# Optimization experiments

Measured on AMD Instinct MI355X. Metric: run time of the kernel, lower is better.

The kernel has to match this reference:

```python
import jax, jax.numpy as jnp
import numpy as np

B, D, H, W, C = 2, 8, 128, 128, 64
HEADS, DH = 4, 16
EPS = 1e-12  # torch F.normalize eps


def setup_inputs() -> dict:
    key = jax.random.key(0)
    ks = jax.random.split(key, 8)
    rn = lambda k, shp, s: jax.random.normal(k, shp, jnp.float32) * s
    return {
        "x_in": rn(ks[0], (B, D, H, W, C), 1.0),
        "Wq": rn(ks[1], (C, HEADS * DH), 0.05),
        "Wk": rn(ks[2], (C, HEADS * DH), 0.05),
        "Wv": rn(ks[3], (C, HEADS * DH), 0.05),
        "rescale": jnp.ones((HEADS, 1, 1), jnp.float32),
        "Wproj": rn(ks[4], (HEADS * DH, C), 0.05),
        "bproj": jnp.zeros((C,), jnp.float32),
        "Wpos1": rn(ks[5], (C, 1, 3, 3, 3), 0.1),
        "Wpos2": rn(ks[6], (C, 1, 3, 3, 3), 0.1),
    }


def _l2norm(x):
    # torch F.normalize(p=2, dim=-1): x / max(||x||, eps)
    return x / jnp.maximum(jnp.linalg.norm(x, axis=-1, keepdims=True), EPS)


def _dwconv3d(x, w):
    # depthwise Conv3d, kernel 3, stride 1, padding 1, groups = channels
    return jax.lax.conv_general_dilated(
        x, w, (1, 1, 1), 'SAME',
        dimension_numbers=('NCDHW', 'OIDHW', 'NCDHW'),
        feature_group_count=w.shape[0])


def reference(x_in, Wq, Wk, Wv, rescale, Wproj, bproj, Wpos1, Wpos2):
    b, d, h, w, c = x_in.shape
    n = d * h * w
    x = x_in.reshape(b, n, c)
    v_inp = x @ Wv                                   # [b, n, heads*dh]
    # [b, heads, dh, n] layout (attention over channel dim)
    q = jnp.transpose((x @ Wq).reshape(b, n, HEADS, DH), (0, 2, 3, 1))
    k = jnp.transpose((x @ Wk).reshape(b, n, HEADS, DH), (0, 2, 3, 1))
    v = jnp.transpose(v_inp.reshape(b, n, HEADS, DH), (0, 2, 3, 1))
    q = _l2norm(q)
    k = _l2norm(k)
    attn = jnp.einsum('bhdn,bhen->bhde', k, q) * rescale  # [b, heads, dh, dh]
    attn = jax.nn.softmax(attn, axis=-1)
    out = jnp.einsum('bhde,bhen->bhdn', attn, v)          # [b, heads, dh, n]
    out = jnp.transpose(out, (0, 3, 1, 2)).reshape(b, n, HEADS * DH)
    out_c = (out @ Wproj + bproj).reshape(b, d, h, w, c)
    # positional branch: depthwise conv -> GELU -> depthwise conv on v_inp
    vv = jnp.transpose(v_inp.reshape(b, d, h, w, c), (0, 4, 1, 2, 3))  # NCDHW
    p = _dwconv3d(vv, Wpos1)
    p = jax.nn.gelu(p, approximate=False)
    p = _dwconv3d(p, Wpos2)
    out_p = jnp.transpose(p, (0, 2, 3, 4, 1))
    return out_c + out_p
```

## Files before the change

### kernel.cpp

```cpp
#include <hip/hip_runtime.h>
#include <math.h>

#define DD 8
#define HH 128
#define WW2 128
#define NPT 131072
#define NTOT 262144
#define NBK 8

typedef __attribute__((ext_vector_type(8))) short short8;
typedef __attribute__((ext_vector_type(4))) float f32x4;
typedef __attribute__((ext_vector_type(4))) unsigned short u16x4;
typedef __attribute__((ext_vector_type(8))) unsigned short u16x8;
typedef unsigned short u16;

static const size_t OFF_P1  = 0;
static const size_t OFF_P2  = 33554432;
static const size_t OFF_V   = 67108864;
static const size_t OFF_PW  = 100663296;
static const size_t OFF_PM  = 100687872;
static const size_t OFF_FLAG= 100704256;
static const size_t OFF_CW  = 100704768;
static const size_t OFF_PART= 134217728;
static const size_t OFF_VP  = 150994944;
#define SP_F    0
#define WQ_F    65536
#define WK_F    69632
#define CW_WPROJ 0
#define CW_WPOS1 4096
#define CW_WPOS2 5824
#define CW_RESC  7552
#define CW_BPROJ 7556

__device__ __forceinline__ float bf2f(u16 u){
  unsigned int x = ((unsigned int)u) << 16;
  return __builtin_bit_cast(float, x);
}
__device__ __forceinline__ u16 f2bf(float f){
  unsigned int x = __builtin_bit_cast(unsigned int, f);
  unsigned int r = (x + 0x7fffu + ((x >> 16) & 1u)) >> 16;
  return (u16)r;
}

__device__ __forceinline__ float fgelu(float o){
  float z  = o * 0.70710678118654752f;
  float az = fabsf(z);
  float t1 = __builtin_amdgcn_rcpf(fmaf(0.3275911f, az, 1.f));
  float poly = t1 * fmaf(t1, fmaf(t1, fmaf(t1, fmaf(t1, 1.061405429f,
               -1.453152027f), 1.421413741f), -0.284496736f), 0.254829592f);
  float ex = __expf(-z * z);
  float er = 1.f - poly * ex;
  er = (z < 0.f) ? -er : er;
  return 0.5f * o * (1.f + er);
}

__device__ __forceinline__ int probe_isf32(const void* x, int t){
  u16 u = ((const u16*)x)[2 * (t & 63)];
  int e = (u >> 7) & 0xFF;
  int plaus = (u == 0) || (u == 0x8000u) || (e >= 100 && e <= 130);
  unsigned long long m = __ballot(plaus);
  return (__popcll(m) < 48) ? 1 : 0;
}

__global__ __launch_bounds__(256) void k_prep(const void* __restrict__ x,
    const void* __restrict__ Wproj, const void* __restrict__ rescale,
    const void* __restrict__ bproj, const void* __restrict__ Wpos1,
    const void* __restrict__ Wpos2, const void* __restrict__ Wq,
    const void* __restrict__ Wk, const void* __restrict__ Wv,
    int* __restrict__ flag, float* __restrict__ cw, float* __restrict__ gpart,
    u16* __restrict__ packW){
  __shared__ int sflag;
  int t = threadIdx.x, blk = blockIdx.x;
  if (t < 64){
    int f = probe_isf32(x, t);
    if (t == 0) sflag = f;
  }
  __syncthreads();
  int isf32 = sflag;
  if (blk < 32){
    for (int i = blk * 2048 + t; i < (blk + 1) * 2048; i += 256)
      gpart[i] = 0.f;
    if (blk == 0){
      if (t == 0) *flag = isf32;
      auto conv = [&](const void* src, float* dst, int n){
        for (int i = t; i < n; i += 256)
          dst[i] = isf32 ? ((const float*)src)[i] : bf2f(((const u16*)src)[i]);
      };
      conv(Wproj, cw + CW_WPROJ, 4096);
      conv(Wpos1, cw + CW_WPOS1, 1728);
      conv(Wpos2, cw + CW_WPOS2, 1728);
      conv(rescale, cw + CW_RESC, 4);
      conv(bproj,   cw + CW_BPROJ, 64);
      conv(Wq, gpart + WQ_F, 4096);
      conv(Wk, gpart + WK_F, 4096);
    }
  } else {
    int o = (blk - 32) * 256 + t;
    int f = o >> 9, l = (o >> 3) & 63, j = o & 7;
    int tt = f >> 1, s = f & 1;
    int k = s * 32 + (l >> 4) * 8 + j;
    int n = tt * 16 + (l & 15);
    int idx = k * 64 + n;
    float val = isf32 ? ((const float*)Wv)[idx] : bf2f(((const u16*)Wv)[idx]);
    packW[o] = f2bf(val);
  }
}

__device__ __forceinline__ short8 ld8_adapt(const void* p, size_t idx, int isf32){
  if (!isf32) return *(const short8*)((const u16*)p + idx);
  const float4* f = (const float4*)((const float*)p + idx);
  float4 u = f[0], v2 = f[1];
  short8 r;
  r[0] = (short)f2bf(u.x);  r[1] = (short)f2bf(u.y);
  r[2] = (short)f2bf(u.z);  r[3] = (short)f2bf(u.w);
  r[4] = (short)f2bf(v2.x); r[5] = (short)f2bf(v2.y);
  r[6] = (short)f2bf(v2.z); r[7] = (short)f2bf(v2.w);
  return r;
}

__global__ __launch_bounds__(512) void k_qkv(const void* __restrict__ x,
                                             const int* __restrict__ flag,
                                             const u16* __restrict__ packW,
                                             u16* __restrict__ vT,
                                             u16* __restrict__ vP,
                                             float* __restrict__ Sp){
  __shared__ u16 sXT[64][136];
  int isf32 = *flag;
  int wave = threadIdx.x >> 6, lane = threadIdx.x & 63;
  int m = lane & 15, quad = lane >> 4;
  const short8* bw = (const short8*)packW;
  short8 bv[8];
#pragma unroll
  for (int f = 0; f < 8; f++) bv[f] = bw[f * 64 + lane];
  int c1 = wave >> 1, c2p = (wave & 1) * 2;
  f32x4 aS[2];
  aS[0] = (f32x4)(0.f); aS[1] = (f32x4)(0.f);

  int pbase = blockIdx.x * 512;
  int b = pbase >> 17;

  for (int s = 0; s < 4; s++){
    int p0 = pbase + s * 128 + wave * 16;
    size_t rowbase = (size_t)(p0 + m) * 64;
    short8 a0 = ld8_adapt(x, rowbase + quad * 8, isf32);
    short8 a1 = ld8_adapt(x, rowbase + 32 + quad * 8, isf32);
    f32x4 av[4];
#pragma unroll
    for (int t = 0; t < 4; t++) av[t] = (f32x4)(0.f);
#pragma unroll
    for (int t = 0; t < 4; t++){
      av[t] = __builtin_amdgcn_mfma_f32_16x16x32_bf16(a0, bv[t * 2 + 0], av[t], 0, 0, 0);
      av[t] = __builtin_amdgcn_mfma_f32_16x16x32_bf16(a1, bv[t * 2 + 1], av[t], 0, 0, 0);
    }
    int nloc = p0 & (NPT - 1);
#pragma unroll
    for (int t = 0; t < 4; t++){
      u16x4 pk;
#pragma unroll
      for (int r = 0; r < 4; r++) pk[r] = f2bf(av[t][r]);
      *(u16x4*)(vT + ((size_t)(b * 64 + t * 16 + m)) * NPT + nloc + quad * 4) = pk;
#pragma unroll
      for (int r = 0; r < 4; r++)
        vP[(size_t)(p0 + quad * 4 + r) * 64 + t * 16 + m] = pk[r];
    }
    if (s) __syncthreads();
#pragma unroll
    for (int j = 0; j < 8; j++){
      sXT[quad * 8 + j][wave * 16 + m]      = (u16)a0[j];
      sXT[32 + quad * 8 + j][wave * 16 + m] = (u16)a1[j];
    }
    __syncthreads();
#pragma unroll
    for (int ks = 0; ks < 4; ks++){
      short8 fA  = *(const short8*)&sXT[c1 * 16 + m][ks * 32 + quad * 8];
      short8 fB0 = *(const short8*)&sXT[(c2p + 0) * 16 + m][ks * 32 + quad * 8];
      short8 fB1 = *(const short8*)&sXT[(c2p + 1) * 16 + m][ks * 32 + quad * 8];
      aS[0] = __builtin_amdgcn_mfma_f32_16x16x32_bf16(fA, fB0, aS[0], 0, 0, 0);
      aS[1] = __builtin_amdgcn_mfma_f32_16x16x32_bf16(fA, fB1, aS[1], 0, 0, 0);
    }
  }
  int bk = blockIdx.x & (NBK - 1);
  float* Sb = Sp + (size_t)(bk * 2 + b) * 4096;
#pragma unroll
  for (int tt = 0; tt < 2; tt++)
#pragma unroll
    for (int r = 0; r < 4; r++)
      atomicAdd(&Sb[(c1 * 16 + quad * 4 + r) * 64 + (c2p + tt) * 16 + m], aS[tt][r]);
}

__global__ __launch_bounds__(256) void k_attn_h(const float* __restrict__ Sp,
    const float* __restrict__ wqk, const float* __restrict__ cw,
    u16* __restrict__ packM){
  __shared__ float sS[64 * 65];
  __shared__ float sWh[1024];
  __shared__ float sT[1024];
  __shared__ float sG[256];
  __shared__ float sA[256];
  __shared__ float sNq[16], sNk[16];
  int blk = blockIdx.x, t = threadIdx.x;
  int b = blk >> 2, h = blk & 3;
  for (int i = t; i < 4096; i += 256){
    float s = 0.f;
#pragma unroll
    for (int bk = 0; bk < NBK; bk++) s += Sp[(size_t)(bk * 2 + b) * 4096 + i];
    sS[(i >> 6) * 65 + (i & 63)] = s;
  }
  for (int i = t; i < 1024; i += 256)
    sWh[i] = wqk[(i >> 4) * 64 + h * 16 + (i & 15)];
  __syncthreads();
  int cc = t & 63, eg = t >> 6;
  {
    float a0 = 0.f, a1 = 0.f, a2 = 0.f, a3 = 0.f;
    for (int c2 = 0; c2 < 64; c2++){
      float sv = sS[cc * 65 + c2];
      a0 = fmaf(sv, sWh[c2 * 16 + eg * 4 + 0], a0);
      a1 = fmaf(sv, sWh[c2 * 16 + eg * 4 + 1], a1);
      a2 = fmaf(sv, sWh[c2 * 16 + eg * 4 + 2], a2);
      a3 = fmaf(sv, sWh[c2 * 16 + eg * 4 + 3], a3);
    }
    sT[cc * 16 + eg * 4 + 0] = a0;
    sT[cc * 16 + eg * 4 + 1] = a1;
    sT[cc * 16 + eg * 4 + 2] = a2;
    sT[cc * 16 + eg * 4 + 3] = a3;
  }
  __syncthreads();
  if (t < 16){
    float a = 0.f;
    for (int c = 0; c < 64; c++) a += sWh[c * 16 + t] * sT[c * 16 + t];
    sNq[t] = a;
  }
  __syncthreads();
  for (int i = t; i < 1024; i += 256)
    sWh[i] = wqk[4096 + (i >> 4) * 64 + h * 16 + (i & 15)];
  __syncthreads();
  {
    int d = t >> 4, e = t & 15;
    float a = 0.f;
    for (int c = 0; c < 64; c++) a += sWh[c * 16 + d] * sT[c * 16 + e];
    sG[d * 16 + e] = a;
  }
  __syncthreads();
  {
    float a0 = 0.f, a1 = 0.f, a2 = 0.f, a3 = 0.f;
    for (int c2 = 0; c2 < 64; c2++){
      float sv = sS[cc * 65 + c2];
      a0 = fmaf(sv, sWh[c2 * 16 + eg * 4 + 0], a0);
      a1 = fmaf(sv, sWh[c2 * 16 + eg * 4 + 1], a1);
      a2 = fmaf(sv, sWh[c2 * 16 + eg * 4 + 2], a2);
      a3 = fmaf(sv, sWh[c2 * 16 + eg * 4 + 3], a3);
    }
    __syncthreads();
    sT[cc * 16 + eg * 4 + 0] = a0;
    sT[cc * 16 + eg * 4 + 1] = a1;
    sT[cc * 16 + eg * 4 + 2] = a2;
    sT[cc * 16 + eg * 4 + 3] = a3;
  }
  __syncthreads();
  if (t < 16){
    float a = 0.f;
    for (int c = 0; c < 64; c++) a += sWh[c * 16 + t] * sT[c * 16 + t];
    sNk[t] = a;
  }
  __syncthreads();
  for (int i = t; i < 1024; i += 256)
    sT[i] = cw[CW_WPROJ + (h * 16 + (i >> 6)) * 64 + (i & 63)];
  if (t < 16){
    int d = t;
    float nk = fmaxf(sqrtf(sNk[d]), 1e-12f);
    float rs = cw[CW_RESC + h];
    float lg[16]; float mx = -1e30f;
#pragma unroll
    for (int e = 0; e < 16; e++){
      float nq = fmaxf(sqrtf(sNq[e]), 1e-12f);
      float L = sG[d * 16 + e] / (nk * nq) * rs;
      lg[e] = L; mx = fmaxf(mx, L);
    }
    float sum = 0.f;
#pragma unroll
    for (int e = 0; e < 16; e++){ lg[e] = expf(lg[e] - mx); sum += lg[e]; }
    float inv = 1.f / sum;
#pragma unroll
    for (int e = 0; e < 16; e++) sA[d * 16 + e] = lg[e] * inv;
  }
  __syncthreads();
#pragma unroll
  for (int q = 0; q < 4; q++){
    int i = q * 256 + t;
    int t4 = i >> 8, lhi = (i >> 7) & 1, llo = (i >> 3) & 15, j = i & 7;
    int e = lhi * 8 + j, c = t4 * 16 + llo;
    float acc = 0.f;
#pragma unroll
    for (int d = 0; d < 16; d++) acc += sA[d * 16 + e] * sT[d * 64 + c];
    int f = t4 * 2 + (h >> 1);
    int l = (2 * (h & 1) + lhi) * 16 + llo;
    packM[b * 4096 + f * 512 + l * 8 + j] = f2bf(acc);
  }
}

template <bool GELU>
__global__ __launch_bounds__(256, 3) void k_dwconv(const u16* __restrict__ src,
    const float* __restrict__ wpos, u16* __restrict__ dst){
  int xi = threadIdx.x & 15, ty = threadIdx.x >> 4;
  int zp = ty >> 2, yq = ty & 3;
  int x0 = xi * 8;
  int c  = blockIdx.x;
  int y0 = blockIdx.y * 8 + yq * 2;
  int b  = blockIdx.z;
  int z0 = zp * 2;
  const float* wg = wpos + c * 27;
  float w27[27];
#pragma unroll
  for (int i = 0; i < 27; i++) w27[i] = wg[i];
  const u16* plane = src + (size_t)(b * 64 + c) * NPT;

  short8 raw[16];
  float  msk[16];
#pragma unroll
  for (int iz = 0; iz < 4; iz++){
    int zz = z0 - 1 + iz;
    int zc = zz < 0 ? 0 : (zz > DD - 1 ? DD - 1 : zz);
    float zm = (zz == zc) ? 1.f : 0.f;
#pragma unroll
    for (int iy = 0; iy < 4; iy++){
      int yy = y0 - 1 + iy;
      int yc = yy < 0 ? 0 : (yy > HH - 1 ? HH - 1 : yy);
      raw[iz * 4 + iy] = *(const short8*)(plane + zc * 16384 + yc * 128 + x0);
      msk[iz * 4 + iy] = zm * ((yy == yc) ? 1.f : 0.f);
    }
  }

  float acc[2][2][8];
#pragma unroll
  for (int dz = 0; dz < 2; dz++)
#pragma unroll
    for (int dy = 0; dy < 2; dy++)
#pragma unroll
      for (int xx = 0; xx < 8; xx++) acc[dz][dy][xx] = 0.f;

#pragma unroll
  for (int iz = 0; iz < 4; iz++){
#pragma unroll
    for (int iy = 0; iy < 4; iy++){
      short8 mid = raw[iz * 4 + iy];
      float m = msk[iz * 4 + iy];
      float row[10];
#pragma unroll
      for (int e = 0; e < 8; e++) row[1 + e] = bf2f((u16)mid[e]);
      float lf = __shfl_up(row[8], 1);
      float rg = __shfl_down(row[1], 1);
      row[0] = (xi > 0)  ? lf : 0.f;
      row[9] = (xi < 15) ? rg : 0.f;
#pragma unroll
      for (int e = 0; e < 10; e++) row[e] *= m;
#pragma unroll
      for (int dzi = 0; dzi < 2; dzi++){
        int kd = iz - dzi;
        if (kd < 0 || kd > 2) continue;
#pragma unroll
        for (int dyi = 0; dyi < 2; dyi++){
          int kh = iy - dyi;
          if (kh < 0 || kh > 2) continue;
#pragma unroll
          for (int kw = 0; kw < 3; kw++){
            float w = w27[kd * 9 + kh * 3 + kw];
#pragma unroll
            for (int xx = 0; xx < 8; xx++)
              acc[dzi][dyi][xx] = fmaf(row[xx + kw], w, acc[dzi][dyi][xx]);
          }
        }
      }
    }
  }
#pragma unroll
  for (int dzi = 0; dzi < 2; dzi++){
    int zo = z0 + dzi;
#pragma unroll
    for (int dyi = 0; dyi < 2; dyi++){
      int yo = y0 + dyi;
      u16x8 pk;
#pragma unroll
      for (int xx = 0; xx < 8; xx++){
        float o = acc[dzi][dyi][xx];
        if (GELU) o = fgelu(o);
        pk[xx] = f2bf(o);
      }
      *(u16x8*)(dst + (size_t)(b * 64 + c) * NPT + zo * 16384 + yo * 128 + x0) = pk;
    }
  }
}

__global__ __launch_bounds__(256) void k_final(const u16* __restrict__ vP,
                                               const u16* __restrict__ packM,
                                               const float* __restrict__ bprojf,
                                               const u16* __restrict__ p2T,
                                               float* __restrict__ out){
  int wave = threadIdx.x >> 6, lane = threadIdx.x & 63;
  int m = lane & 15, quad = lane >> 4;
  int p0 = blockIdx.x * 64 + wave * 16;
  int b = p0 >> 17;
  int nloc = p0 & (NPT - 1);
  size_t rowbase = (size_t)(p0 + m) * 64;
  short8 a0 = *(const short8*)(vP + rowbase + quad * 8);
  short8 a1 = *(const short8*)(vP + rowbase + 32 + quad * 8);
  const short8* bm = (const short8*)(packM + (size_t)b * 4096);
  f32x4 acc[4];
#pragma unroll
  for (int t = 0; t < 4; t++) acc[t] = (f32x4)(0.f);
#pragma unroll
  for (int t = 0; t < 4; t++){
    short8 b0 = bm[(t * 2 + 0) * 64 + lane];
    short8 b1 = bm[(t * 2 + 1) * 64 + lane];
    acc[t] = __builtin_amdgcn_mfma_f32_16x16x32_bf16(a0, b0, acc[t], 0, 0, 0);
    acc[t] = __builtin_amdgcn_mfma_f32_16x16x32_bf16(a1, b1, acc[t], 0, 0, 0);
  }
#pragma unroll
  for (int t = 0; t < 4; t++){
    int c = t * 16 + m;
    float bias = bprojf[c];
    u16x4 pv = *(const u16x4*)(p2T + (size_t)(b * 64 + c) * NPT + nloc + quad * 4);
#pragma unroll
    for (int r = 0; r < 4; r++){
      size_t p = (size_t)p0 + quad * 4 + r;
      out[p * 64 + c] = acc[t][r] + bias + bf2f(pv[r]);
    }
  }
}

extern "C" void kernel_launch(void* const* d_in, const int* in_sizes, int n_in,
                              void* d_out, int out_size, void* d_ws, size_t ws_size,
                              hipStream_t stream){
  (void)in_sizes; (void)n_in; (void)out_size; (void)ws_size;
  const void* x      = d_in[0];
  const void* Wq     = d_in[1];
  const void* Wk     = d_in[2];
  const void* Wv     = d_in[3];
  const void* rescale= d_in[4];
  const void* Wproj  = d_in[5];
  const void* bproj  = d_in[6];
  const void* Wpos1  = d_in[7];
  const void* Wpos2  = d_in[8];

  char* ws = (char*)d_ws;
  u16* p1T   = (u16*)(ws + OFF_P1);
  u16* p2T   = (u16*)(ws + OFF_P2);
  u16* vT    = (u16*)(ws + OFF_V);
  u16* vP    = (u16*)(ws + OFF_VP);
  u16* packW = (u16*)(ws + OFF_PW);
  u16* packM = (u16*)(ws + OFF_PM);
  int* flag  = (int*)(ws + OFF_FLAG);
  float* cw  = (float*)(ws + OFF_CW);
  float* part= (float*)(ws + OFF_PART);
  float* Sp  = part + SP_F;
  float* wqk = part + WQ_F;
  float* out = (float*)d_out;

  k_prep<<<48, 256, 0, stream>>>(x, Wproj, rescale, bproj, Wpos1, Wpos2, Wq, Wk, Wv,
                                 flag, cw, Sp, packW);
  k_qkv<<<NTOT / 512, 512, 0, stream>>>(x, flag, packW, vT, vP, Sp);
  k_attn_h<<<8, 256, 0, stream>>>(Sp, wqk, cw, packM);
  k_dwconv<true><<<dim3(64, 16, 2), 256, 0, stream>>>(vT, cw + CW_WPOS1, p1T);
  k_dwconv<false><<<dim3(64, 16, 2), 256, 0, stream>>>(p1T, cw + CW_WPOS2, p2T);
  k_final<<<NTOT / 64, 256, 0, stream>>>(vP, packM, cw + CW_BPROJ, p2T, out);
}
```

Baseline: 264.4 us.

## Fuse both depthwise convs into one kernel via LDS halo tile; coalesce vP stores

```diff
diff --git a/kernel.cpp b/kernel.cpp
--- a/kernel.cpp
+++ b/kernel.cpp
@@ -125,6 +125,7 @@
                                              u16* __restrict__ vP,
                                              float* __restrict__ Sp){
   __shared__ u16 sXT[64][136];
+  __shared__ u16 sV[8][16][72];
   int isf32 = *flag;
   int wave = threadIdx.x >> 6, lane = threadIdx.x & 63;
   int m = lane & 15, quad = lane >> 4;
@@ -160,8 +161,14 @@
       for (int r = 0; r < 4; r++) pk[r] = f2bf(av[t][r]);
       *(u16x4*)(vT + ((size_t)(b * 64 + t * 16 + m)) * NPT + nloc + quad * 4) = pk;
 #pragma unroll
-      for (int r = 0; r < 4; r++)
-        vP[(size_t)(p0 + quad * 4 + r) * 64 + t * 16 + m] = pk[r];
+      for (int r = 0; r < 4; r++) sV[wave][quad * 4 + r][t * 16 + m] = pk[r];
+    }
+    {
+      int pr = lane >> 3, ch8 = (lane & 7) * 8;
+      u16x8 v0 = *(const u16x8*)&sV[wave][pr][ch8];
+      *(u16x8*)(vP + (size_t)(p0 + pr) * 64 + ch8) = v0;
+      u16x8 v1 = *(const u16x8*)&sV[wave][8 + pr][ch8];
+      *(u16x8*)(vP + (size_t)(p0 + 8 + pr) * 64 + ch8) = v1;
     }
     if (s) __syncthreads();
 #pragma unroll
@@ -297,95 +304,140 @@
   }
 }
 
-template <bool GELU>
-__global__ __launch_bounds__(256, 3) void k_dwconv(const u16* __restrict__ src,
-    const float* __restrict__ wpos, u16* __restrict__ dst){
+__global__ __launch_bounds__(256, 3) void k_convf(const u16* __restrict__ src,
+    const float* __restrict__ wpos1, const float* __restrict__ wpos2,
+    u16* __restrict__ dst){
+  __shared__ float sP[8][10][132];
   int xi = threadIdx.x & 15, ty = threadIdx.x >> 4;
-  int zp = ty >> 2, yq = ty & 3;
   int x0 = xi * 8;
   int c  = blockIdx.x;
-  int y0 = blockIdx.y * 8 + yq * 2;
+  int y0 = blockIdx.y * 8;
   int b  = blockIdx.z;
-  int z0 = zp * 2;
-  const float* wg = wpos + c * 27;
-  float w27[27];
-#pragma unroll
-  for (int i = 0; i < 27; i++) w27[i] = wg[i];
+  int z  = ty >> 1;
+  int yh = ty & 1;
   const u16* plane = src + (size_t)(b * 64 + c) * NPT;
-
-  short8 raw[16];
-  float  msk[16];
-#pragma unroll
-  for (int iz = 0; iz < 4; iz++){
-    int zz = z0 - 1 + iz;
-    int zc = zz < 0 ? 0 : (zz > DD - 1 ? DD - 1 : zz);
-    float zm = (zz == zc) ? 1.f : 0.f;
-#pragma unroll
-    for (int iy = 0; iy < 4; iy++){
-      int yy = y0 - 1 + iy;
-      int yc = yy < 0 ? 0 : (yy > HH - 1 ? HH - 1 : yy);
-      raw[iz * 4 + iy] = *(const short8*)(plane + zc * 16384 + yc * 128 + x0);
-      msk[iz * 4 + iy] = zm * ((yy == yc) ? 1.f : 0.f);
-    }
-  }
-
-  float acc[2][2][8];
-#pragma unroll
-  for (int dz = 0; dz < 2; dz++)
-#pragma unroll
-    for (int dy = 0; dy < 2; dy++)
-#pragma unroll
-      for (int xx = 0; xx < 8; xx++) acc[dz][dy][xx] = 0.f;
-
-#pragma unroll
-  for (int iz = 0; iz < 4; iz++){
-#pragma unroll
-    for (int iy = 0; iy < 4; iy++){
-      short8 mid = raw[iz * 4 + iy];
-      float m = msk[iz * 4 + iy];
-      float row[10];
-#pragma unroll
-      for (int e = 0; e < 8; e++) row[1 + e] = bf2f((u16)mid[e]);
-      float lf = __shfl_up(row[8], 1);
-      float rg = __shfl_down(row[1], 1);
-      row[0] = (xi > 0)  ? lf : 0.f;
-      row[9] = (xi < 15) ? rg : 0.f;
-#pragma unroll
-      for (int e = 0; e < 10; e++) row[e] *= m;
-#pragma unroll
-      for (int dzi = 0; dzi < 2; dzi++){
-        int kd = iz - dzi;
-        if (kd < 0 || kd > 2) continue;
-#pragma unroll
-        for (int dyi = 0; dyi < 2; dyi++){
-          int kh = iy - dyi;
+  float w1[27];
+#pragma unroll
+  for (int i = 0; i < 27; i++) w1[i] = wpos1[c * 27 + i];
+
+  int ybase = y0 - 1 + yh * 5;
+  float acc1[5][8];
+#pragma unroll
+  for (int o = 0; o < 5; o++)
+#pragma unroll
+    for (int xx = 0; xx < 8; xx++) acc1[o][xx] = 0.f;
+
+#pragma unroll
+  for (int half = 0; half < 2; half++){
+    const int iy0 = half ? 4 : 0, niy = half ? 3 : 4;
+    short8 raw[12]; float msk[12];
+#pragma unroll
+    for (int ii = 0; ii < 4; ii++){
+      if (ii >= niy) break;
+      int iy = iy0 + ii;
+      int ay = ybase - 1 + iy;
+      int ayc = ay < 0 ? 0 : (ay > HH - 1 ? HH - 1 : ay);
+      float ym = (ay == ayc) ? 1.f : 0.f;
+#pragma unroll
+      for (int kd = 0; kd < 3; kd++){
+        int az = z - 1 + kd;
+        int azc = az < 0 ? 0 : (az > DD - 1 ? DD - 1 : az);
+        float zm = (az == azc) ? 1.f : 0.f;
+        raw[ii * 3 + kd] = *(const short8*)(plane + azc * 16384 + ayc * 128 + x0);
+        msk[ii * 3 + kd] = ym * zm;
+      }
+    }
+#pragma unroll
+    for (int ii = 0; ii < 4; ii++){
+      if (ii >= niy) break;
+      int iy = iy0 + ii;
+#pragma unroll
+      for (int kd = 0; kd < 3; kd++){
+        short8 mid = raw[ii * 3 + kd];
+        float m = msk[ii * 3 + kd];
+        float row[10];
+#pragma unroll
+        for (int e = 0; e < 8; e++) row[1 + e] = bf2f((u16)mid[e]);
+        float lf = __shfl_up(row[8], 1);
+        float rg = __shfl_down(row[1], 1);
+        row[0] = (xi > 0)  ? lf : 0.f;
+        row[9] = (xi < 15) ? rg : 0.f;
+#pragma unroll
+        for (int e = 0; e < 10; e++) row[e] *= m;
+#pragma unroll
+        for (int o = 0; o < 5; o++){
+          int kh = iy - o;
           if (kh < 0 || kh > 2) continue;
 #pragma unroll
           for (int kw = 0; kw < 3; kw++){
-            float w = w27[kd * 9 + kh * 3 + kw];
+            float w = w1[kd * 9 + kh * 3 + kw];
 #pragma unroll
             for (int xx = 0; xx < 8; xx++)
-              acc[dzi][dyi][xx] = fmaf(row[xx + kw], w, acc[dzi][dyi][xx]);
+              acc1[o][xx] = fmaf(row[xx + kw], w, acc1[o][xx]);
           }
         }
       }
     }
   }
 #pragma unroll
-  for (int dzi = 0; dzi < 2; dzi++){
-    int zo = z0 + dzi;
-#pragma unroll
-    for (int dyi = 0; dyi < 2; dyi++){
-      int yo = y0 + dyi;
-      u16x8 pk;
-#pragma unroll
-      for (int xx = 0; xx < 8; xx++){
-        float o = acc[dzi][dyi][xx];
-        if (GELU) o = fgelu(o);
-        pk[xx] = f2bf(o);
+  for (int o = 0; o < 5; o++){
+    int ay = ybase + o;
+    float vm = (ay >= 0 && ay < HH) ? 1.f : 0.f;
+    int lrow = yh * 5 + o;
+#pragma unroll
+    for (int xx = 0; xx < 8; xx++)
+      sP[z][lrow][1 + x0 + xx] = fgelu(acc1[o][xx]) * vm;
+    if (xi == 0)  sP[z][lrow][0]   = 0.f;
+    if (xi == 15) sP[z][lrow][129] = 0.f;
+  }
+  __syncthreads();
+
+  float w2[27];
+#pragma unroll
+  for (int i = 0; i < 27; i++) w2[i] = wpos2[c * 27 + i];
+  int yq = yh * 4;
+  float acc2[4][8];
+#pragma unroll
+  for (int r = 0; r < 4; r++)
+#pragma unroll
+    for (int xx = 0; xx < 8; xx++) acc2[r][xx] = 0.f;
+
+#pragma unroll
+  for (int kd = 0; kd < 3; kd++){
+    int az = z - 1 + kd;
+    int azc = az < 0 ? 0 : (az > DD - 1 ? DD - 1 : az);
+    float zm = (az == azc) ? 1.f : 0.f;
+#pragma unroll
+    for (int ily = 0; ily < 6; ily++){
+      int ly = yq + ily;
+      const float* rp = &sP[azc][ly][x0];
+      float4 f0 = *(const float4*)rp;
+      float4 f1 = *(const float4*)(rp + 4);
+      float rb[10];
+      rb[0] = f0.x; rb[1] = f0.y; rb[2] = f0.z; rb[3] = f0.w;
+      rb[4] = f1.x; rb[5] = f1.y; rb[6] = f1.z; rb[7] = f1.w;
+      rb[8] = rp[8]; rb[9] = rp[9];
+#pragma unroll
+      for (int r = 0; r < 4; r++){
+        int kh = ily - r;
+        if (kh < 0 || kh > 2) continue;
+#pragma unroll
+        for (int kw = 0; kw < 3; kw++){
+          float w = w2[kd * 9 + kh * 3 + kw] * zm;
+#pragma unroll
+          for (int xx = 0; xx < 8; xx++)
+            acc2[r][xx] = fmaf(rb[xx + kw], w, acc2[r][xx]);
+        }
       }
-      *(u16x8*)(dst + (size_t)(b * 64 + c) * NPT + zo * 16384 + yo * 128 + x0) = pk;
-    }
+    }
+  }
+#pragma unroll
+  for (int r = 0; r < 4; r++){
+    u16x8 pk;
+#pragma unroll
+    for (int xx = 0; xx < 8; xx++) pk[xx] = f2bf(acc2[r][xx]);
+    *(u16x8*)(dst + (size_t)(b * 64 + c) * NPT + z * 16384 +
+              (size_t)(y0 + yq + r) * 128 + x0) = pk;
   }
 }
 
@@ -441,7 +493,6 @@
   const void* Wpos2  = d_in[8];
 
   char* ws = (char*)d_ws;
-  u16* p1T   = (u16*)(ws + OFF_P1);
   u16* p2T   = (u16*)(ws + OFF_P2);
   u16* vT    = (u16*)(ws + OFF_V);
   u16* vP    = (u16*)(ws + OFF_VP);
@@ -458,7 +509,6 @@
                                  flag, cw, Sp, packW);
   k_qkv<<<NTOT / 512, 512, 0, stream>>>(x, flag, packW, vT, vP, Sp);
   k_attn_h<<<8, 256, 0, stream>>>(Sp, wqk, cw, packM);
-  k_dwconv<true><<<dim3(64, 16, 2), 256, 0, stream>>>(vT, cw + CW_WPOS1, p1T);
-  k_dwconv<false><<<dim3(64, 16, 2), 256, 0, stream>>>(p1T, cw + CW_WPOS2, p2T);
+  k_convf<<<dim3(64, 16, 2), 256, 0, stream>>>(vT, cw + CW_WPOS1, cw + CW_WPOS2, p2T);
   k_final<<<NTOT / 64, 256, 0, stream>>>(vP, packM, cw + CW_BPROJ, p2T, out);
 }
```

Result: slower. 305.3 us (+15.5%).
